# Kernel tuning notes

Hardware: AMD Instinct MI355X
Metric: run time of the kernel (lower is better)

Reference implementation:

```python
import jax, jax.numpy as jnp
import numpy as np

NEG_BIG = -9.0e15  # matches torch's -9000000000000000.0 mask fill
ALPHA = 0.2        # leakyrelu negative slope


def setup_inputs() -> dict:
    key = jax.random.key(0)
    k1, k2, k3, k4, k5 = jax.random.split(key, 5)
    N, F_in, F_out = 4096, 512, 64
    stdv = 1.0 / np.sqrt(F_out)
    x = jax.random.normal(k1, (N, F_in), dtype=jnp.float32)
    adj = jax.random.randint(k2, (N, N), 0, 2, dtype=jnp.int32)
    W = jax.random.uniform(k3, (F_in, F_out), dtype=jnp.float32, minval=-stdv, maxval=stdv)
    a = jax.random.normal(k4, (2 * F_out, 1), dtype=jnp.float32) * 0.1
    bias = jax.random.uniform(k5, (F_out,), dtype=jnp.float32, minval=-stdv, maxval=stdv)
    return {"x": x, "adj": adj, "W": W, "a": a, "bias": bias}


def _gat_forward(x, adj, W, a, bias):
    N = x.shape[0]
    F_out = W.shape[1]
    h = x @ W  # (N, F)
    a1 = a[:F_out, 0]   # weights hitting the first concat half
    a2 = a[F_out:, 0]   # weights hitting the second concat half
    # First half: row k=i*N+j of the concat holds h_j  ->  e1[j] = h_j . a1
    e1 = h @ a1  # (N,)
    # Second half of this repo's concat is NOT h_i; exact index algebra:
    # second[k=i*N+j, r] = h[(r*N+i)//F, (((r*N+i)%F)*N + j) % F]
    # Since it depends on j only via j % F, build table T[i, t] (t = j % F).
    r = jnp.arange(F_out)[:, None]          # (F, 1)
    i = jnp.arange(N)[None, :]              # (1, N)
    m = r * N + i                           # (F, N)
    p = m // F_out                          # row index into h
    s0 = m % F_out
    t = jnp.arange(F_out)                   # (F,)
    col = (s0[..., None] * N + t) % F_out   # (F, N, F) column index into h
    vals = h[p[..., None], col]             # (F, N, F)
    T = jnp.einsum('r,rit->it', a2, vals)   # (N, F)
    j = jnp.arange(N)
    e2 = T[:, j % F_out]                    # (N, N) second-half contribution
    e = e1[None, :] + e2                    # (N, N) pre-activation scores
    e = jnp.where(e > 0, e, ALPHA * e)      # LeakyReLU(0.2)
    e = jnp.where(adj > 0, e, NEG_BIG)      # mask non-edges
    att = jax.nn.softmax(e, axis=1)         # row-wise softmax (dropout = eval identity)
    out = jax.nn.relu(att @ h) + bias       # relu BEFORE bias add, as in source
    return out


def reference(x, adj, W, a, bias):
    return _gat_forward(x, adj, W, a, bias)
```

## Files before the change

kernel.cpp:

```cpp
#include <hip/hip_runtime.h>
#include <math.h>

#define N_NODES 4096
#define F_IN    512
#define F_OUT   64
#define ALPHA   0.2f
#define NPART   8

typedef _Float16 half8 __attribute__((ext_vector_type(8)));
typedef _Float16 half4 __attribute__((ext_vector_type(4)));
typedef float    floatx4 __attribute__((ext_vector_type(4)));

union H8U4 { half8 h; uint32_t u[4]; };

__device__ __forceinline__ void async_copy16(void* lds, const void* g) {
    __builtin_amdgcn_global_load_lds(
        (const __attribute__((address_space(1))) unsigned int*)g,
        (__attribute__((address_space(3))) unsigned int*)lds, 16, 0, 0);
}

__global__ __launch_bounds__(512) void k_pre(const float* __restrict__ x,
                                             const int* __restrict__ adj,
                                             const float* __restrict__ W,
                                             const float* __restrict__ a,
                                             uint32_t* __restrict__ bm,
                                             float* __restrict__ h,
                                             _Float16* __restrict__ hT,
                                             float* __restrict__ e1) {
    __shared__ float red[8][16][64];
    int gb  = blockIdx.x;
    int tid = threadIdx.x;

    if (gb < 1024) {
        int wid = gb * 512 + tid;
        const int* p = adj + (size_t)wid * 32;
        uint32_t m = 0;
#pragma unroll
        for (int q = 0; q < 8; ++q) {
            int4 v = *(const int4*)(p + q * 4);
            m |= (v.x > 0 ? 1u : 0u) << (q * 4 + 0);
            m |= (v.y > 0 ? 1u : 0u) << (q * 4 + 1);
            m |= (v.z > 0 ? 1u : 0u) << (q * 4 + 2);
            m |= (v.w > 0 ? 1u : 0u) << (q * 4 + 3);
        }
        bm[wid] = m;
        return;
    }

    int lane = tid & 63;
    int w    = tid >> 6;
    int i0   = (gb - 1024) * 16;
    int n    = lane & 15;
    int quad = lane >> 4;

    floatx4 acc[4] = {{0,0,0,0},{0,0,0,0},{0,0,0,0},{0,0,0,0}};

    const float* xr = x + (size_t)(i0 + n) * F_IN + w * 64 + quad * 8;
#pragma unroll
    for (int kk = 0; kk < 64; kk += 32) {
        float4 x0 = *(const float4*)(xr + kk);
        float4 x1 = *(const float4*)(xr + kk + 4);
        half8 af = {(_Float16)x0.x, (_Float16)x0.y, (_Float16)x0.z, (_Float16)x0.w,
                    (_Float16)x1.x, (_Float16)x1.y, (_Float16)x1.z, (_Float16)x1.w};
        int k0 = w * 64 + kk + quad * 8;
#pragma unroll
        for (int g = 0; g < 4; ++g) {
            const float* wc = W + (size_t)k0 * F_OUT + g * 16 + n;
            half8 bf = {(_Float16)wc[0 * 64], (_Float16)wc[1 * 64], (_Float16)wc[2 * 64], (_Float16)wc[3 * 64],
                        (_Float16)wc[4 * 64], (_Float16)wc[5 * 64], (_Float16)wc[6 * 64], (_Float16)wc[7 * 64]};
            acc[g] = __builtin_amdgcn_mfma_f32_16x16x32_f16(af, bf, acc[g], 0, 0, 0);
        }
    }
#pragma unroll
    for (int g = 0; g < 4; ++g)
#pragma unroll
        for (int r = 0; r < 4; ++r)
            red[w][g * 4 + r][lane] = acc[g][r];
    __syncthreads();
    if (w != 0) return;
#pragma unroll
    for (int g = 0; g < 4; ++g)
#pragma unroll
        for (int r = 0; r < 4; ++r) {
            float v = 0.f;
#pragma unroll
            for (int ww = 0; ww < 8; ++ww)
                v += red[ww][g * 4 + r][lane];
            acc[g][r] = v;
        }
#pragma unroll
    for (int g = 0; g < 4; ++g) {
        half4 hv;
#pragma unroll
        for (int r = 0; r < 4; ++r) {
            h[(size_t)(i0 + quad * 4 + r) * F_OUT + g * 16 + n] = acc[g][r];
            hv[r] = (_Float16)acc[g][r];
        }
        *(half4*)(hT + (size_t)(g * 16 + n) * N_NODES + i0 + quad * 4) = hv;
    }
    float a1v[4];
#pragma unroll
    for (int g = 0; g < 4; ++g) a1v[g] = a[g * 16 + n];
#pragma unroll
    for (int r = 0; r < 4; ++r) {
        float v = acc[0][r] * a1v[0] + acc[1][r] * a1v[1] + acc[2][r] * a1v[2] + acc[3][r] * a1v[3];
        v += __shfl_xor(v, 1, 64);
        v += __shfl_xor(v, 2, 64);
        v += __shfl_xor(v, 4, 64);
        v += __shfl_xor(v, 8, 64);
        if (n == 0) e1[i0 + quad * 4 + r] = v;
    }
}

__global__ __launch_bounds__(256, 2) void k_main(const uint32_t* __restrict__ bm,
                                                 const float* __restrict__ h,
                                                 const float* __restrict__ e1,
                                                 const float* __restrict__ a,
                                                 const _Float16* __restrict__ hT,
                                                 float* __restrict__ out_part,
                                                 float* __restrict__ den_part) {
    __shared__ _Float16 lds_B[4][16][512];
    __shared__ _Float16 lds_P[512];
    __shared__ float    lds_part[4][64];
    __shared__ float    TqS[64];

    int tid  = threadIdx.x;
    int lane = tid & 63;
    int w    = tid >> 6;
    int b    = blockIdx.x;
    int rb   = b >> 3;
    int s    = b & 7;
    int i0   = rb * 64 + w * 16;
    int n    = lane & 15;
    int quad = lane >> 4;

#pragma unroll
    for (int it = 0; it < 4; ++it) {
        int jb = s * 512 + it * 128;
        const _Float16* hT_base = hT + (size_t)(w * 16 + n) * N_NODES + jb + quad * 8;
#pragma unroll
        for (int c = 0; c < 4; ++c)
            async_copy16(&lds_B[it][w * 4 + c][0], hT_base + c * 32);
    }

    const uint32_t* bmr = bm + (size_t)(i0 + n) * (N_NODES / 32) + s * 16;
    uint4 bwa = *(const uint4*)(bmr + 0);
    uint4 bwb = *(const uint4*)(bmr + 4);
    uint4 bwc = *(const uint4*)(bmr + 8);
    uint4 bwd = *(const uint4*)(bmr + 12);
    uint32_t bw[16] = {bwa.x, bwa.y, bwa.z, bwa.w, bwb.x, bwb.y, bwb.z, bwb.w,
                       bwc.x, bwc.y, bwc.z, bwc.w, bwd.x, bwd.y, bwd.z, bwd.w};

    {
        int t  = tid & 63;
        int rp = tid >> 6;
        const float* a2 = a + F_OUT;
        float ssum = 0.f;
#pragma unroll
        for (int rr = 0; rr < 16; ++rr) {
            int r = rp * 16 + rr;
            ssum += a2[r] * h[(size_t)r * 4096 + rb * 64 + t];
        }
        lds_part[rp][t] = ssum;
    }
    __syncthreads();
    if (tid < 64)
        TqS[tid] = lds_part[0][tid] + lds_part[1][tid] + lds_part[2][tid] + lds_part[3][tid];
    __syncthreads();
    {
        int j = s * 512 + tid * 2;
        float2 ev = *(const float2*)(e1 + j);
        float e0 = ev.x + TqS[(tid * 2) & 63];
        float e1v = ev.y + TqS[(tid * 2 + 1) & 63];
        e0  = e0  > 0.f ? e0  : ALPHA * e0;
        e1v = e1v > 0.f ? e1v : ALPHA * e1v;
        lds_P[tid * 2]     = (_Float16)__expf(e0);
        lds_P[tid * 2 + 1] = (_Float16)__expf(e1v);
    }
    __syncthreads();

    floatx4 acc[4] = {{0,0,0,0},{0,0,0,0},{0,0,0,0},{0,0,0,0}};
    floatx4 accd = {0, 0, 0, 0};
    _Float16 one_h = (n == 0) ? (_Float16)1.0f : (_Float16)0.0f;
    half8 ones_f = {one_h, one_h, one_h, one_h, one_h, one_h, one_h, one_h};

#pragma unroll
    for (int it = 0; it < 4; ++it) {
#pragma unroll
        for (int c = 0; c < 4; ++c) {
            uint32_t mbyte = bw[it * 4 + c] >> (quad * 8);
            H8U4 pv, af;
            pv.h = *(const half8*)&lds_P[it * 128 + c * 32 + quad * 8];
            af.u[0] = pv.u[0] & (((mbyte &   1u) ? 0x0000FFFFu : 0u) | ((mbyte &   2u) ? 0xFFFF0000u : 0u));
            af.u[1] = pv.u[1] & (((mbyte &   4u) ? 0x0000FFFFu : 0u) | ((mbyte &   8u) ? 0xFFFF0000u : 0u));
            af.u[2] = pv.u[2] & (((mbyte &  16u) ? 0x0000FFFFu : 0u) | ((mbyte &  32u) ? 0xFFFF0000u : 0u));
            af.u[3] = pv.u[3] & (((mbyte &  64u) ? 0x0000FFFFu : 0u) | ((mbyte & 128u) ? 0xFFFF0000u : 0u));
#pragma unroll
            for (int g4 = 0; g4 < 4; ++g4) {
                half8 bf = *(const half8*)&lds_B[it][g4 * 4 + c][lane * 8];
                acc[g4] = __builtin_amdgcn_mfma_f32_16x16x32_f16(af.h, bf, acc[g4], 0, 0, 0);
            }
            accd = __builtin_amdgcn_mfma_f32_16x16x32_f16(af.h, ones_f, accd, 0, 0, 0);
        }
    }

    float* op = out_part + ((size_t)s * N_NODES + i0) * F_OUT;
#pragma unroll
    for (int g4 = 0; g4 < 4; ++g4)
#pragma unroll
        for (int r = 0; r < 4; ++r)
            op[(quad * 4 + r) * F_OUT + g4 * 16 + n] = acc[g4][r];
    if (n == 0) {
#pragma unroll
        for (int r = 0; r < 4; ++r)
            den_part[s * N_NODES + i0 + quad * 4 + r] = accd[r];
    }
}

__global__ __launch_bounds__(128) void k_out(const float* __restrict__ out_part,
                                             const float* __restrict__ den_part,
                                             const float* __restrict__ bias,
                                             float* __restrict__ out) {
    int idx4 = blockIdx.x * 128 + threadIdx.x;
    int base = idx4 * 4;
    int i = base >> 6;
    int t = base & 63;
    float4 sacc = {0.f, 0.f, 0.f, 0.f};
    float dacc = 0.f;
#pragma unroll
    for (int p = 0; p < NPART; ++p) {
        float4 v = ((const float4*)(out_part + (size_t)p * N_NODES * F_OUT))[idx4];
        sacc.x += v.x; sacc.y += v.y; sacc.z += v.z; sacc.w += v.w;
        dacc += den_part[p * N_NODES + i];
    }
    float4 bv = *(const float4*)(bias + t);
    float4 o;
    o.x = fmaxf(sacc.x / dacc, 0.f) + bv.x;
    o.y = fmaxf(sacc.y / dacc, 0.f) + bv.y;
    o.z = fmaxf(sacc.z / dacc, 0.f) + bv.z;
    o.w = fmaxf(sacc.w / dacc, 0.f) + bv.w;
    ((float4*)out)[idx4] = o;
}

extern "C" void kernel_launch(void* const* d_in, const int* in_sizes, int n_in,
                              void* d_out, int out_size, void* d_ws, size_t ws_size,
                              hipStream_t stream) {
    const float* x    = (const float*)d_in[0];
    const int*   adj  = (const int*)d_in[1];
    const float* W    = (const float*)d_in[2];
    const float* a    = (const float*)d_in[3];
    const float* bias = (const float*)d_in[4];
    float* out = (float*)d_out;

    char* ws = (char*)d_ws;
    float*    h        = (float*)ws;
    _Float16* hT       = (_Float16*)(ws + 1024 * 1024);
    float*    e1       = (float*)(ws + 1536 * 1024);
    uint32_t* bm       = (uint32_t*)(ws + 2128 * 1024);
    float*    out_part = (float*)(ws + 4176 * 1024);
    float*    den_part = (float*)(ws + (4176 + 8192) * 1024);

    k_pre <<<1280, 512, 0, stream>>>(x, adj, W, a, bm, h, hT, e1);
    k_main<<<512, 256, 0, stream>>>(bm, h, e1, a, hT, out_part, den_part);
    k_out <<<512, 128, 0, stream>>>(out_part, den_part, bias, out);
}
```

Baseline: 120.9 us.

## Double split-K partitions and read hT directly from global instead of LDS

Splits the attention-times-h reduction into 16 column partitions instead of 8, so the main kernel launches 1024 blocks that each cover 256 columns, with a launch bound allowing 4 blocks per CU. The async global-to-LDS staging of hT is removed and the MFMA B operands are loaded straight from global memory, which drops the large LDS buffer and raises occupancy. The cost is twice the partial-output traffic for the reduction kernel, plus B fragments now coming through the cache hierarchy rather than shared memory. Workspace offsets are moved to make room for the larger partial buffers.

```diff
diff --git a/kernel.cpp b/kernel.cpp
--- a/kernel.cpp
+++ b/kernel.cpp
@@ -5,19 +5,13 @@
 #define F_IN    512
 #define F_OUT   64
 #define ALPHA   0.2f
-#define NPART   8
+#define NPART   16
 
 typedef _Float16 half8 __attribute__((ext_vector_type(8)));
 typedef _Float16 half4 __attribute__((ext_vector_type(4)));
 typedef float    floatx4 __attribute__((ext_vector_type(4)));
 
 union H8U4 { half8 h; uint32_t u[4]; };
-
-__device__ __forceinline__ void async_copy16(void* lds, const void* g) {
-    __builtin_amdgcn_global_load_lds(
-        (const __attribute__((address_space(1))) unsigned int*)g,
-        (__attribute__((address_space(3))) unsigned int*)lds, 16, 0, 0);
-}
 
 __global__ __launch_bounds__(512) void k_pre(const float* __restrict__ x,
                                              const int* __restrict__ adj,
@@ -112,15 +106,14 @@
     }
 }
 
-__global__ __launch_bounds__(256, 2) void k_main(const uint32_t* __restrict__ bm,
-                                                 const float* __restrict__ h,
-                                                 const float* __restrict__ e1,
-                                                 const float* __restrict__ a,
-                                                 const _Float16* __restrict__ hT,
-                                                 float* __restrict__ out_part,
-                                                 float* __restrict__ den_part) {
-    __shared__ _Float16 lds_B[4][16][512];
-    __shared__ _Float16 lds_P[512];
+__global__ __launch_bounds__(256, 4) void k_main3(const uint32_t* __restrict__ bm,
+                                                  const float* __restrict__ h,
+                                                  const float* __restrict__ e1,
+                                                  const float* __restrict__ a,
+                                                  const _Float16* __restrict__ hT,
+                                                  float* __restrict__ out_part,
+                                                  float* __restrict__ den_part) {
+    __shared__ _Float16 lds_P[256];
     __shared__ float    lds_part[4][64];
     __shared__ float    TqS[64];
 
@@ -128,28 +121,16 @@
     int lane = tid & 63;
     int w    = tid >> 6;
     int b    = blockIdx.x;
-    int rb   = b >> 3;
-    int s    = b & 7;
+    int rb   = b >> 4;
+    int s    = b & 15;
     int i0   = rb * 64 + w * 16;
     int n    = lane & 15;
     int quad = lane >> 4;
 
-#pragma unroll
-    for (int it = 0; it < 4; ++it) {
-        int jb = s * 512 + it * 128;
-        const _Float16* hT_base = hT + (size_t)(w * 16 + n) * N_NODES + jb + quad * 8;
-#pragma unroll
-        for (int c = 0; c < 4; ++c)
-            async_copy16(&lds_B[it][w * 4 + c][0], hT_base + c * 32);
-    }
-
-    const uint32_t* bmr = bm + (size_t)(i0 + n) * (N_NODES / 32) + s * 16;
+    const uint32_t* bmr = bm + (size_t)(i0 + n) * (N_NODES / 32) + s * 8;
     uint4 bwa = *(const uint4*)(bmr + 0);
     uint4 bwb = *(const uint4*)(bmr + 4);
-    uint4 bwc = *(const uint4*)(bmr + 8);
-    uint4 bwd = *(const uint4*)(bmr + 12);
-    uint32_t bw[16] = {bwa.x, bwa.y, bwa.z, bwa.w, bwb.x, bwb.y, bwb.z, bwb.w,
-                       bwc.x, bwc.y, bwc.z, bwc.w, bwd.x, bwd.y, bwd.z, bwd.w};
+    uint32_t bw[8] = {bwa.x, bwa.y, bwa.z, bwa.w, bwb.x, bwb.y, bwb.z, bwb.w};
 
     {
         int t  = tid & 63;
@@ -168,14 +149,10 @@
         TqS[tid] = lds_part[0][tid] + lds_part[1][tid] + lds_part[2][tid] + lds_part[3][tid];
     __syncthreads();
     {
-        int j = s * 512 + tid * 2;
-        float2 ev = *(const float2*)(e1 + j);
-        float e0 = ev.x + TqS[(tid * 2) & 63];
-        float e1v = ev.y + TqS[(tid * 2 + 1) & 63];
-        e0  = e0  > 0.f ? e0  : ALPHA * e0;
-        e1v = e1v > 0.f ? e1v : ALPHA * e1v;
-        lds_P[tid * 2]     = (_Float16)__expf(e0);
-        lds_P[tid * 2 + 1] = (_Float16)__expf(e1v);
+        int j = s * 256 + tid;
+        float e0 = e1[j] + TqS[tid & 63];
+        e0 = e0 > 0.f ? e0 : ALPHA * e0;
+        lds_P[tid] = (_Float16)__expf(e0);
     }
     __syncthreads();
 
@@ -184,24 +161,22 @@
     _Float16 one_h = (n == 0) ? (_Float16)1.0f : (_Float16)0.0f;
     half8 ones_f = {one_h, one_h, one_h, one_h, one_h, one_h, one_h, one_h};
 
-#pragma unroll
-    for (int it = 0; it < 4; ++it) {
-#pragma unroll
-        for (int c = 0; c < 4; ++c) {
-            uint32_t mbyte = bw[it * 4 + c] >> (quad * 8);
-            H8U4 pv, af;
-            pv.h = *(const half8*)&lds_P[it * 128 + c * 32 + quad * 8];
-            af.u[0] = pv.u[0] & (((mbyte &   1u) ? 0x0000FFFFu : 0u) | ((mbyte &   2u) ? 0xFFFF0000u : 0u));
-            af.u[1] = pv.u[1] & (((mbyte &   4u) ? 0x0000FFFFu : 0u) | ((mbyte &   8u) ? 0xFFFF0000u : 0u));
-            af.u[2] = pv.u[2] & (((mbyte &  16u) ? 0x0000FFFFu : 0u) | ((mbyte &  32u) ? 0xFFFF0000u : 0u));
-            af.u[3] = pv.u[3] & (((mbyte &  64u) ? 0x0000FFFFu : 0u) | ((mbyte & 128u) ? 0xFFFF0000u : 0u));
-#pragma unroll
-            for (int g4 = 0; g4 < 4; ++g4) {
-                half8 bf = *(const half8*)&lds_B[it][g4 * 4 + c][lane * 8];
-                acc[g4] = __builtin_amdgcn_mfma_f32_16x16x32_f16(af.h, bf, acc[g4], 0, 0, 0);
-            }
-            accd = __builtin_amdgcn_mfma_f32_16x16x32_f16(af.h, ones_f, accd, 0, 0, 0);
-        }
+    const int jb = s * 256;
+#pragma unroll
+    for (int c = 0; c < 8; ++c) {
+        uint32_t mbyte = bw[c] >> (quad * 8);
+        H8U4 pv, af;
+        pv.h = *(const half8*)&lds_P[c * 32 + quad * 8];
+        af.u[0] = pv.u[0] & (((mbyte &   1u) ? 0x0000FFFFu : 0u) | ((mbyte &   2u) ? 0xFFFF0000u : 0u));
+        af.u[1] = pv.u[1] & (((mbyte &   4u) ? 0x0000FFFFu : 0u) | ((mbyte &   8u) ? 0xFFFF0000u : 0u));
+        af.u[2] = pv.u[2] & (((mbyte &  16u) ? 0x0000FFFFu : 0u) | ((mbyte &  32u) ? 0xFFFF0000u : 0u));
+        af.u[3] = pv.u[3] & (((mbyte &  64u) ? 0x0000FFFFu : 0u) | ((mbyte & 128u) ? 0xFFFF0000u : 0u));
+#pragma unroll
+        for (int g4 = 0; g4 < 4; ++g4) {
+            half8 bf = *(const half8*)(hT + (size_t)(g4 * 16 + n) * N_NODES + jb + c * 32 + quad * 8);
+            acc[g4] = __builtin_amdgcn_mfma_f32_16x16x32_f16(af.h, bf, acc[g4], 0, 0, 0);
+        }
+        accd = __builtin_amdgcn_mfma_f32_16x16x32_f16(af.h, ones_f, accd, 0, 0, 0);
     }
 
     float* op = out_part + ((size_t)s * N_NODES + i0) * F_OUT;
@@ -256,11 +231,11 @@
     float*    h        = (float*)ws;
     _Float16* hT       = (_Float16*)(ws + 1024 * 1024);
     float*    e1       = (float*)(ws + 1536 * 1024);
-    uint32_t* bm       = (uint32_t*)(ws + 2128 * 1024);
-    float*    out_part = (float*)(ws + 4176 * 1024);
-    float*    den_part = (float*)(ws + (4176 + 8192) * 1024);
-
-    k_pre <<<1280, 512, 0, stream>>>(x, adj, W, a, bm, h, hT, e1);
-    k_main<<<512, 256, 0, stream>>>(bm, h, e1, a, hT, out_part, den_part);
-    k_out <<<512, 128, 0, stream>>>(out_part, den_part, bias, out);
-}
+    uint32_t* bm       = (uint32_t*)(ws + 2176 * 1024);
+    float*    out_part = (float*)(ws + 4224 * 1024);
+    float*    den_part = (float*)(ws + (4224 + 16384) * 1024);
+
+    k_pre  <<<1280, 512, 0, stream>>>(x, adj, W, a, bm, h, hT, e1);
+    k_main3<<<1024, 256, 0, stream>>>(bm, h, e1, a, hT, out_part, den_part);
+    k_out  <<<512, 128, 0, stream>>>(out_part, den_part, bias, out);
+}
```

New measurement: 135.1 us. 11.7% more time.
